# Kernel tuning notes

Hardware: AMD Instinct MI355X
Metric: run time of the kernel (lower is better)

## Reference

```python
import jax, jax.numpy as jnp
import numpy as np

B, S = 2, 1024
IN, OUT = 1024, 1024
N_IN, N_OUT = 32, 32          # isqrt(IN), isqrt(OUT)
CD = 64                       # compressed_feature_dim
K = 2                         # num_monarchs
D1 = N_IN * N_IN * N_OUT      # 32768, flat M1 size per token
D2 = N_OUT * N_IN * N_OUT     # 32768, flat M2 size per token


def setup_inputs() -> dict:
    key = jax.random.key(0)
    ks = jax.random.split(key, 13)
    g = lambda k, shape, s=0.02: jax.random.normal(k, shape, dtype=jnp.float32) * s
    return {
        "x":  jax.random.normal(ks[0], (B, S, IN), dtype=jnp.float32),
        "Wc": g(ks[1], (IN, CD)),  "bc": g(ks[2], (CD,)),
        "W1": g(ks[3], (K, CD, D1)), "b1": g(ks[4], (K, D1)),
        "W2": g(ks[5], (K, CD, D2)), "b2": g(ks[6], (K, D2)),
        "Wm": g(ks[7], (CD, K)),   "bm": g(ks[8], (K,)),
        "Wb": g(ks[9], (CD, OUT)), "bb": g(ks[10], (OUT,)),
        "Wr": g(ks[11], (CD, 1)),  "br": g(ks[12], (1,)),
    }


def reference(x, Wc, bc, W1, b1, W2, b2, Wm, bm, Wb, bb, Wr, br):
    b, s, _ = x.shape
    # compressor: Linear + Tanh -> [B,S,CD]
    cf = jnp.tanh(x @ Wc + bc)
    # per-expert generated flat weights: [B,S,K,D]
    gen1 = jnp.einsum('bsc,kcd->bskd', cf, W1) + b1
    gen2 = jnp.einsum('bsc,kcd->bskd', cf, W2) + b2
    # expert mixing coefficients -> softmax over K
    coeffs = jax.nn.softmax(cf @ Wm + bm, axis=-1)  # [B,S,K]
    M1f = jnp.einsum('bskd,bsk->bsd', gen1, coeffs)
    M2f = jnp.einsum('bskd,bsk->bsd', gen2, coeffs)
    # Monarch block matmul with per-token weights
    M1 = M1f.reshape(b, s, N_IN, N_IN, N_OUT)   # g=N_IN blocks of [N_IN,N_OUT]
    M2 = M2f.reshape(b, s, N_OUT, N_IN, N_OUT)  # g=N_OUT blocks of [N_IN,N_OUT]
    x1 = x.reshape(b, s, N_IN, N_IN)
    h1 = jnp.einsum('bsgi,bsgio->bsgo', x1, M1)      # [B,S,N_IN,N_OUT]
    h1t = jnp.swapaxes(h1, -1, -2)                   # [B,S,N_OUT,N_IN]
    h2 = jnp.einsum('bsgi,bsgio->bsgo', h1t, M2)     # [B,S,N_OUT,N_OUT]
    y = h2.reshape(b, s, OUT)
    # per-token scale and bias
    ratio = cf @ Wr + br                             # [B,S,1]
    bias = cf @ Wb + bb                              # [B,S,OUT]
    return y * ratio + bias
```

## Files before the change

### kernel.cpp

```cpp
#include <hip/hip_runtime.h>
#include <cstddef>

typedef unsigned short ushortT;
typedef short s8v __attribute__((ext_vector_type(8)));
typedef float f32x4 __attribute__((ext_vector_type(4)));

constexpr int NTOK = 2048;

__device__ inline ushortT f2bf(float f) {
  unsigned u = __float_as_uint(f);
  u += 0x7fffu + ((u >> 16) & 1u);
  return (ushortT)(u >> 16);
}

__global__ __launch_bounds__(256) void prep_kernel(
    const float* __restrict__ x, const float* __restrict__ Wc, const float* __restrict__ bc,
    const float* __restrict__ Wm, const float* __restrict__ bm,
    const float* __restrict__ Wr, const float* __restrict__ br,
    ushortT* __restrict__ FP, float* __restrict__ ratio)
{
  const int tid = threadIdx.x;
  const int c = tid & 63;
  const int q = tid >> 6;
  const int t0 = blockIdx.x * 8;
  __shared__ float part[4][8][64];
  __shared__ float cf_s[8][64];
  __shared__ float a0s[8], a1s[8];

  float acc[8];
#pragma unroll
  for (int p = 0; p < 8; ++p) acc[p] = 0.f;

  const float* xq = x + (size_t)t0 * 1024 + q * 256;
  const float* wq = Wc + (size_t)(q * 256) * 64 + c;
#pragma unroll 4
  for (int jj = 0; jj < 64; ++jj) {
    float w0 = wq[(jj * 4 + 0) * 64];
    float w1 = wq[(jj * 4 + 1) * 64];
    float w2 = wq[(jj * 4 + 2) * 64];
    float w3 = wq[(jj * 4 + 3) * 64];
#pragma unroll
    for (int p = 0; p < 8; ++p) {
      float4 xv = *(const float4*)(xq + (size_t)p * 1024 + jj * 4);
      acc[p] = fmaf(xv.x, w0, acc[p]);
      acc[p] = fmaf(xv.y, w1, acc[p]);
      acc[p] = fmaf(xv.z, w2, acc[p]);
      acc[p] = fmaf(xv.w, w3, acc[p]);
    }
  }
#pragma unroll
  for (int p = 0; p < 8; ++p) part[q][p][c] = acc[p];
  __syncthreads();

#pragma unroll
  for (int r = 0; r < 2; ++r) {
    int idx = tid + r * 256;
    int p = idx >> 6, cc = idx & 63;
    float s = part[0][p][cc] + part[1][p][cc] + part[2][p][cc] + part[3][p][cc] + bc[cc];
    cf_s[p][cc] = tanhf(s);
  }
  __syncthreads();

#pragma unroll 1
  for (int pp = 0; pp < 2; ++pp) {
    int p = q * 2 + pp;
    float cf = cf_s[p][c];
    float z0 = cf * Wm[2 * c], z1 = cf * Wm[2 * c + 1], rr = cf * Wr[c];
    for (int off = 32; off; off >>= 1) {
      z0 += __shfl_down(z0, off);
      z1 += __shfl_down(z1, off);
      rr += __shfl_down(rr, off);
    }
    if (c == 0) {
      z0 += bm[0]; z1 += bm[1];
      float mx = fmaxf(z0, z1);
      float e0 = expf(z0 - mx), e1 = expf(z1 - mx);
      float a0 = e0 / (e0 + e1);
      a0s[p] = a0;
      a1s[p] = 1.0f - a0;
      ratio[t0 + p] = rr + br[0];
    }
  }
  __syncthreads();

  const int ks0 = c >> 5, kk = c & 31;
  const int slot = (kk >> 3) * 16, e = kk & 7;
#pragma unroll
  for (int pp = 0; pp < 2; ++pp) {
    int p = q * 2 + pp;
    int t = t0 + p, tt = t >> 4, tok = t & 15;
    size_t base = (size_t)tt * 2560;
    float cf = cf_s[p][c];
    float a0 = a0s[p], a1 = a1s[p];
    FP[base + (size_t)ks0 * 512 + (slot + tok) * 8 + e]       = f2bf(a0 * cf);
    FP[base + (size_t)(2 + ks0) * 512 + (slot + tok) * 8 + e] = f2bf(a1 * cf);
    if (c < 32) {
      float v = (c == 0) ? a0 : (c == 1) ? a1 : 0.0f;
      FP[base + 4 * 512 + ((c >> 3) * 16 + tok) * 8 + (c & 7)] = f2bf(v);
    }
  }
}

__global__ __launch_bounds__(256) void pack_w_kernel(
    const float* __restrict__ W1, const float* __restrict__ b1,
    const float* __restrict__ W2, const float* __restrict__ b2,
    const float* __restrict__ Wb, const float* __restrict__ bb,
    ushortT* __restrict__ P1, ushortT* __restrict__ P2, ushortT* __restrict__ WbP)
{
  const int g = blockIdx.x, jc = blockIdx.y, fac = blockIdx.z;
  if (fac == 2 && g != 0) return;
  const float* W  = (fac == 0) ? W1 : W2;
  const float* bv = (fac == 0) ? b1 : b2;
  ushortT* P = (fac == 0) ? P1 : (fac == 1) ? P2 : WbP;
  const int tid = threadIdx.x;
  __shared__ ushortT lds[16][1024];

#pragma unroll
  for (int it = 0; it < 16; ++it) {
    int idx = tid + it * 256;
    int rl = idx >> 8, c4 = idx & 255;
    int jj = jc * 16 + rl;
    float4 v = make_float4(0.f, 0.f, 0.f, 0.f);
    if (fac < 2) {
      if (jj < 128)       v = *(const float4*)(W  + (size_t)jj * 32768 + g * 1024 + c4 * 4);
      else if (jj < 130)  v = *(const float4*)(bv + (size_t)(jj - 128) * 32768 + g * 1024 + c4 * 4);
    } else {
      if (jj < 128)       v = *(const float4*)(Wb + (size_t)(jj & 63) * 1024 + c4 * 4);
      else if (jj < 130)  v = *(const float4*)(bb + c4 * 4);
    }
    int col0 = c4 * 4;
    int sw = col0 ^ ((col0 >> 4) & 0x1C);
    ushortT* d = &lds[rl][sw];
    d[0] = f2bf(v.x); d[1] = f2bf(v.y); d[2] = f2bf(v.z); d[3] = f2bf(v.w);
  }
  __syncthreads();
  const int ks = jc >> 1, kh = jc & 1;
#pragma unroll
  for (int it = 0; it < 8; ++it) {
    int idx = tid + it * 256;
    int ct_l = idx >> 5, kkg_l = (idx >> 4) & 1, cl = idx & 15;
    int scol;
    if (fac < 2) {
      int o = ct_l >> 1, ib = (ct_l & 1) * 16;
      scol = (ib + cl) * 32 + o;
    } else {
      scol = ct_l * 16 + cl;
    }
    scol ^= ((scol >> 4) & 0x1C);
    int r0 = kkg_l * 8;
    ushortT v[8];
#pragma unroll
    for (int e = 0; e < 8; ++e) v[e] = lds[r0 + e][scol];
    int kkg = kh * 2 + kkg_l;
    size_t ctile = (fac < 2) ? (size_t)(g * 64 + ct_l) : (size_t)ct_l;
    size_t off = ctile * 2560 + (size_t)ks * 512 + (kkg * 16 + cl) * 8;
    uint4 qv;
    qv.x = v[0] | ((unsigned)v[1] << 16);
    qv.y = v[2] | ((unsigned)v[3] << 16);
    qv.z = v[4] | ((unsigned)v[5] << 16);
    qv.w = v[6] | ((unsigned)v[7] << 16);
    *(uint4*)(P + off) = qv;
  }
}

__global__ __launch_bounds__(256) void tr_kernel(
    const float* __restrict__ h1, float* __restrict__ h1x)
{
  __shared__ float lds[8 * 1061];
  const int tid = threadIdx.x, t0 = blockIdx.x * 8;
#pragma unroll
  for (int it = 0; it < 8; ++it) {
    int idx = tid + it * 256;
    int r = idx >> 8, c4 = idx & 255;
    float4 v = *(const float4*)(h1 + (size_t)(t0 + r) * 1024 + c4 * 4);
    int cc = c4 * 4, i = cc >> 5, b0 = cc & 31;
    float* d = lds + r * 1061 + i * 33 + b0;
    d[0] = v.x; d[1] = v.y; d[2] = v.z; d[3] = v.w;
  }
  __syncthreads();
#pragma unroll
  for (int it = 0; it < 8; ++it) {
    int idx = tid + it * 256;
    int g = idx >> 6, rest = idx & 63, r = rest >> 3, i4 = rest & 7;
    float4 v;
    v.x = lds[r * 1061 + (i4 * 4 + 0) * 33 + g];
    v.y = lds[r * 1061 + (i4 * 4 + 1) * 33 + g];
    v.z = lds[r * 1061 + (i4 * 4 + 2) * 33 + g];
    v.w = lds[r * 1061 + (i4 * 4 + 3) * 33 + g];
    *(float4*)(h1x + (size_t)g * 65536 + (size_t)(t0 + r) * 32 + i4 * 4) = v;
  }
}

template <int PASS>
__global__ __launch_bounds__(256, 2) void mm_kernel(
    const s8v* __restrict__ fP, const s8v* __restrict__ wP,
    const s8v* __restrict__ wbP,
    const float* __restrict__ xg,
    const float* __restrict__ rat,
    float* __restrict__ outp)
{
  __shared__ s8v bsh[2][1280];
  __shared__ float xs[2][64][33];
  __shared__ float hs[2][64][9];
  __shared__ float bls[2][64][9];
  const int tid = threadIdx.x;
  const int lane = tid & 63;
  const int w = tid >> 6;
  const int bid = blockIdx.x;
  const int cb  = (bid & 7) * 16 + (bid >> 6);
  const int tbg = (bid >> 3) & 7;
  const int g = cb >> 2;

  const s8v* ap = wP + (size_t)(cb * 16 + w * 4) * 320 + lane;
  s8v a[4][5];
#pragma unroll
  for (int i = 0; i < 4; ++i)
#pragma unroll
    for (int ks = 0; ks < 5; ++ks) a[i][ks] = ap[i * 320 + ks * 64];

  s8v ab[5];
  if (PASS == 2) {
    const s8v* abp = wbP + (size_t)(cb >> 1) * 320 + lane;
#pragma unroll
    for (int ks = 0; ks < 5; ++ks) ab[ks] = abp[ks * 64];
  }

  const s8v* fbase = fP + (size_t)(tbg * 4) * 1280;

#pragma unroll
  for (int it = 0; it < 5; ++it) bsh[0][tid + it * 256] = fbase[tid + it * 256];
  __syncthreads();

#pragma unroll 1
  for (int tt2 = 0; tt2 < 4; ++tt2) {
    const int buf = tt2 & 1;
    const int t0 = (tbg * 4 + tt2) * 64;

    float4 xv[2];
#pragma unroll
    for (int it = 0; it < 2; ++it) {
      int idx = tid + it * 256;
      int t = idx >> 3, i4 = idx & 7;
      if (PASS == 1) xv[it] = *(const float4*)(xg + (size_t)(t0 + t) * 1024 + g * 32 + i4 * 4);
      else           xv[it] = *(const float4*)(xg + (size_t)g * 65536 + (size_t)(t0 + t) * 32 + i4 * 4);
    }
    s8v st0, st1, st2, st3, st4;
    if (tt2 < 3) {
      const s8v* fn = fbase + (size_t)(tt2 + 1) * 1280;
      st0 = fn[tid];       st1 = fn[tid + 256]; st2 = fn[tid + 512];
      st3 = fn[tid + 768]; st4 = fn[tid + 1024];
    }

    f32x4 acc[4][4];
#pragma unroll
    for (int i = 0; i < 4; ++i)
#pragma unroll
      for (int j = 0; j < 4; ++j) acc[i][j] = {0.f, 0.f, 0.f, 0.f};
    f32x4 accb = {0.f, 0.f, 0.f, 0.f};

#pragma unroll
    for (int ks = 0; ks < 5; ++ks) {
      s8v b0 = bsh[buf][0 * 320 + ks * 64 + lane];
      s8v b1 = bsh[buf][1 * 320 + ks * 64 + lane];
      s8v b2 = bsh[buf][2 * 320 + ks * 64 + lane];
      s8v b3 = bsh[buf][3 * 320 + ks * 64 + lane];
      if (PASS == 2) {
        s8v bw = bsh[buf][w * 320 + ks * 64 + lane];
        accb = __builtin_amdgcn_mfma_f32_16x16x32_bf16(ab[ks], bw, accb, 0, 0, 0);
      }
#pragma unroll
      for (int i = 0; i < 4; ++i) {
        acc[i][0] = __builtin_amdgcn_mfma_f32_16x16x32_bf16(a[i][ks], b0, acc[i][0], 0, 0, 0);
        acc[i][1] = __builtin_amdgcn_mfma_f32_16x16x32_bf16(a[i][ks], b1, acc[i][1], 0, 0, 0);
        acc[i][2] = __builtin_amdgcn_mfma_f32_16x16x32_bf16(a[i][ks], b2, acc[i][2], 0, 0, 0);
        acc[i][3] = __builtin_amdgcn_mfma_f32_16x16x32_bf16(a[i][ks], b3, acc[i][3], 0, 0, 0);
      }
    }

#pragma unroll
    for (int it = 0; it < 2; ++it) {
      int idx = tid + it * 256;
      int t = idx >> 3, i4 = idx & 7;
      float* d = &xs[buf][t][i4 * 4];
      d[0] = xv[it].x; d[1] = xv[it].y; d[2] = xv[it].z; d[3] = xv[it].w;
    }
    if (tt2 < 3) {
      s8v* dn = &bsh[buf ^ 1][0];
      dn[tid] = st0;        dn[tid + 256] = st1; dn[tid + 512] = st2;
      dn[tid + 768] = st3;  dn[tid + 1024] = st4;
    }
    __syncthreads();

    const int tau = lane & 15, q = lane >> 4;
#pragma unroll
    for (int tt = 0; tt < 4; ++tt) {
      int tl = tt * 16 + tau;
#pragma unroll
      for (int run = 0; run < 2; ++run) {
        float sacc = 0.f;
#pragma unroll
        for (int ch = 0; ch < 2; ++ch) {
          int ct = run * 2 + ch;
          const float* xp = &xs[buf][tl][ch * 16 + q * 4];
          f32x4 av = acc[ct][tt];
          sacc += av[0] * xp[0] + av[1] * xp[1] + av[2] * xp[2] + av[3] * xp[3];
        }
        sacc += __shfl_xor(sacc, 16);
        sacc += __shfl_xor(sacc, 32);
        if (lane < 16) hs[buf][tl][w * 2 + run] = sacc;
      }
    }
    if (PASS == 2) {
      if ((lane >> 5) == (cb & 1)) {
        int ol = ((lane >> 4) & 1) * 4;
#pragma unroll
        for (int r = 0; r < 4; ++r) bls[buf][w * 16 + tau][ol + r] = accb[r];
      }
    }
    __syncthreads();

    if (tid < 128) {
      int row = tid >> 1, half = tid & 1;
      int t = t0 + row;
      int col = g * 32 + (cb & 3) * 8 + half * 4;
      float v0 = hs[buf][row][half * 4 + 0], v1 = hs[buf][row][half * 4 + 1];
      float v2 = hs[buf][row][half * 4 + 2], v3 = hs[buf][row][half * 4 + 3];
      float4 o;
      if (PASS == 2) {
        float r = rat[t];
        o.x = fmaf(v0, r, bls[buf][row][half * 4 + 0]);
        o.y = fmaf(v1, r, bls[buf][row][half * 4 + 1]);
        o.z = fmaf(v2, r, bls[buf][row][half * 4 + 2]);
        o.w = fmaf(v3, r, bls[buf][row][half * 4 + 3]);
      } else {
        o.x = v0; o.y = v1; o.z = v2; o.w = v3;
      }
      *(float4*)(outp + (size_t)t * 1024 + col) = o;
    }
  }
}

extern "C" void kernel_launch(void* const* d_in, const int* in_sizes, int n_in,
                              void* d_out, int out_size, void* d_ws, size_t ws_size,
                              hipStream_t stream) {
  const float* x  = (const float*)d_in[0];
  const float* Wc = (const float*)d_in[1];
  const float* bc = (const float*)d_in[2];
  const float* W1 = (const float*)d_in[3];
  const float* b1 = (const float*)d_in[4];
  const float* W2 = (const float*)d_in[5];
  const float* b2 = (const float*)d_in[6];
  const float* Wm = (const float*)d_in[7];
  const float* bm = (const float*)d_in[8];
  const float* Wb = (const float*)d_in[9];
  const float* bb = (const float*)d_in[10];
  const float* Wr = (const float*)d_in[11];
  const float* br = (const float*)d_in[12];
  float* out = (float*)d_out;

  ushortT* P1  = (ushortT*)d_ws;
  ushortT* P2  = P1 + (size_t)2048 * 2560;
  ushortT* WbP = P2 + (size_t)2048 * 2560;
  ushortT* FP  = WbP + (size_t)64 * 2560;
  float* ratio = (float*)(FP + (size_t)128 * 2560);
  float* h1    = ratio + NTOK;
  float* h1x   = h1 + (size_t)NTOK * 1024;

  prep_kernel<<<dim3(256), dim3(256), 0, stream>>>(x, Wc, bc, Wm, bm, Wr, br, FP, ratio);
  pack_w_kernel<<<dim3(32, 10, 3), dim3(256), 0, stream>>>(W1, b1, W2, b2, Wb, bb, P1, P2, WbP);
  mm_kernel<1><<<dim3(1024), dim3(256), 0, stream>>>(
      (const s8v*)FP, (const s8v*)P1, (const s8v*)WbP, x, nullptr, h1);
  tr_kernel<<<dim3(256), dim3(256), 0, stream>>>(h1, h1x);
  mm_kernel<2><<<dim3(1024), dim3(256), 0, stream>>>(
      (const s8v*)FP, (const s8v*)P2, (const s8v*)WbP, h1x, ratio, out);
}
```

Measured before the change: 95.32 us.

## Merge prep and pack kernels, prefetch B tiles with direct global-to-LDS loads

Combines the token prep kernel and the weight packing kernel into a single launch with block-range dispatch, and trims the empty fac=2 blocks from the grid. In the matmul kernel, the next B tile is now staged with global_load_lds builtins straight into the alternate LDS buffer instead of going through registers. The double-buffered xs/hs/bls arrays become single-buffered, which lowers LDS use. The goal is less launch overhead, fewer registers and less LDS traffic. The cost is a more complex kernel, and the async LDS writes depend on the existing barriers for correct ordering.

Result: slower. 98.09 us (+2.9%).

```diff
diff --git a/kernel.cpp b/kernel.cpp
--- a/kernel.cpp
+++ b/kernel.cpp
@@ -13,153 +13,163 @@
   return (ushortT)(u >> 16);
 }
 
-__global__ __launch_bounds__(256) void prep_kernel(
+__device__ inline void gl_lds16(const s8v* g, s8v* l) {
+  __builtin_amdgcn_global_load_lds(
+      (const __attribute__((address_space(1))) unsigned int*)g,
+      (__attribute__((address_space(3))) unsigned int*)l, 16, 0, 0);
+}
+
+__global__ __launch_bounds__(256) void setup_kernel(
     const float* __restrict__ x, const float* __restrict__ Wc, const float* __restrict__ bc,
     const float* __restrict__ Wm, const float* __restrict__ bm,
     const float* __restrict__ Wr, const float* __restrict__ br,
-    ushortT* __restrict__ FP, float* __restrict__ ratio)
-{
-  const int tid = threadIdx.x;
-  const int c = tid & 63;
-  const int q = tid >> 6;
-  const int t0 = blockIdx.x * 8;
-  __shared__ float part[4][8][64];
-  __shared__ float cf_s[8][64];
-  __shared__ float a0s[8], a1s[8];
-
-  float acc[8];
-#pragma unroll
-  for (int p = 0; p < 8; ++p) acc[p] = 0.f;
-
-  const float* xq = x + (size_t)t0 * 1024 + q * 256;
-  const float* wq = Wc + (size_t)(q * 256) * 64 + c;
-#pragma unroll 4
-  for (int jj = 0; jj < 64; ++jj) {
-    float w0 = wq[(jj * 4 + 0) * 64];
-    float w1 = wq[(jj * 4 + 1) * 64];
-    float w2 = wq[(jj * 4 + 2) * 64];
-    float w3 = wq[(jj * 4 + 3) * 64];
-#pragma unroll
-    for (int p = 0; p < 8; ++p) {
-      float4 xv = *(const float4*)(xq + (size_t)p * 1024 + jj * 4);
-      acc[p] = fmaf(xv.x, w0, acc[p]);
-      acc[p] = fmaf(xv.y, w1, acc[p]);
-      acc[p] = fmaf(xv.z, w2, acc[p]);
-      acc[p] = fmaf(xv.w, w3, acc[p]);
-    }
-  }
-#pragma unroll
-  for (int p = 0; p < 8; ++p) part[q][p][c] = acc[p];
-  __syncthreads();
-
-#pragma unroll
-  for (int r = 0; r < 2; ++r) {
-    int idx = tid + r * 256;
-    int p = idx >> 6, cc = idx & 63;
-    float s = part[0][p][cc] + part[1][p][cc] + part[2][p][cc] + part[3][p][cc] + bc[cc];
-    cf_s[p][cc] = tanhf(s);
-  }
-  __syncthreads();
-
-#pragma unroll 1
-  for (int pp = 0; pp < 2; ++pp) {
-    int p = q * 2 + pp;
-    float cf = cf_s[p][c];
-    float z0 = cf * Wm[2 * c], z1 = cf * Wm[2 * c + 1], rr = cf * Wr[c];
-    for (int off = 32; off; off >>= 1) {
-      z0 += __shfl_down(z0, off);
-      z1 += __shfl_down(z1, off);
-      rr += __shfl_down(rr, off);
-    }
-    if (c == 0) {
-      z0 += bm[0]; z1 += bm[1];
-      float mx = fmaxf(z0, z1);
-      float e0 = expf(z0 - mx), e1 = expf(z1 - mx);
-      float a0 = e0 / (e0 + e1);
-      a0s[p] = a0;
-      a1s[p] = 1.0f - a0;
-      ratio[t0 + p] = rr + br[0];
-    }
-  }
-  __syncthreads();
-
-  const int ks0 = c >> 5, kk = c & 31;
-  const int slot = (kk >> 3) * 16, e = kk & 7;
-#pragma unroll
-  for (int pp = 0; pp < 2; ++pp) {
-    int p = q * 2 + pp;
-    int t = t0 + p, tt = t >> 4, tok = t & 15;
-    size_t base = (size_t)tt * 2560;
-    float cf = cf_s[p][c];
-    float a0 = a0s[p], a1 = a1s[p];
-    FP[base + (size_t)ks0 * 512 + (slot + tok) * 8 + e]       = f2bf(a0 * cf);
-    FP[base + (size_t)(2 + ks0) * 512 + (slot + tok) * 8 + e] = f2bf(a1 * cf);
-    if (c < 32) {
-      float v = (c == 0) ? a0 : (c == 1) ? a1 : 0.0f;
-      FP[base + 4 * 512 + ((c >> 3) * 16 + tok) * 8 + (c & 7)] = f2bf(v);
-    }
-  }
-}
-
-__global__ __launch_bounds__(256) void pack_w_kernel(
     const float* __restrict__ W1, const float* __restrict__ b1,
     const float* __restrict__ W2, const float* __restrict__ b2,
     const float* __restrict__ Wb, const float* __restrict__ bb,
+    ushortT* __restrict__ FP, float* __restrict__ ratio,
     ushortT* __restrict__ P1, ushortT* __restrict__ P2, ushortT* __restrict__ WbP)
 {
-  const int g = blockIdx.x, jc = blockIdx.y, fac = blockIdx.z;
-  if (fac == 2 && g != 0) return;
-  const float* W  = (fac == 0) ? W1 : W2;
-  const float* bv = (fac == 0) ? b1 : b2;
-  ushortT* P = (fac == 0) ? P1 : (fac == 1) ? P2 : WbP;
+  __shared__ __align__(16) char smem[32768];
   const int tid = threadIdx.x;
-  __shared__ ushortT lds[16][1024];
-
-#pragma unroll
-  for (int it = 0; it < 16; ++it) {
-    int idx = tid + it * 256;
-    int rl = idx >> 8, c4 = idx & 255;
-    int jj = jc * 16 + rl;
-    float4 v = make_float4(0.f, 0.f, 0.f, 0.f);
-    if (fac < 2) {
-      if (jj < 128)       v = *(const float4*)(W  + (size_t)jj * 32768 + g * 1024 + c4 * 4);
-      else if (jj < 130)  v = *(const float4*)(bv + (size_t)(jj - 128) * 32768 + g * 1024 + c4 * 4);
-    } else {
-      if (jj < 128)       v = *(const float4*)(Wb + (size_t)(jj & 63) * 1024 + c4 * 4);
-      else if (jj < 130)  v = *(const float4*)(bb + c4 * 4);
-    }
-    int col0 = c4 * 4;
-    int sw = col0 ^ ((col0 >> 4) & 0x1C);
-    ushortT* d = &lds[rl][sw];
-    d[0] = f2bf(v.x); d[1] = f2bf(v.y); d[2] = f2bf(v.z); d[3] = f2bf(v.w);
-  }
-  __syncthreads();
-  const int ks = jc >> 1, kh = jc & 1;
-#pragma unroll
-  for (int it = 0; it < 8; ++it) {
-    int idx = tid + it * 256;
-    int ct_l = idx >> 5, kkg_l = (idx >> 4) & 1, cl = idx & 15;
-    int scol;
-    if (fac < 2) {
-      int o = ct_l >> 1, ib = (ct_l & 1) * 16;
-      scol = (ib + cl) * 32 + o;
-    } else {
-      scol = ct_l * 16 + cl;
-    }
-    scol ^= ((scol >> 4) & 0x1C);
-    int r0 = kkg_l * 8;
-    ushortT v[8];
-#pragma unroll
-    for (int e = 0; e < 8; ++e) v[e] = lds[r0 + e][scol];
-    int kkg = kh * 2 + kkg_l;
-    size_t ctile = (fac < 2) ? (size_t)(g * 64 + ct_l) : (size_t)ct_l;
-    size_t off = ctile * 2560 + (size_t)ks * 512 + (kkg * 16 + cl) * 8;
-    uint4 qv;
-    qv.x = v[0] | ((unsigned)v[1] << 16);
-    qv.y = v[2] | ((unsigned)v[3] << 16);
-    qv.z = v[4] | ((unsigned)v[5] << 16);
-    qv.w = v[6] | ((unsigned)v[7] << 16);
-    *(uint4*)(P + off) = qv;
+  const int bid = blockIdx.x;
+
+  if (bid < 256) {
+    float* part = (float*)smem;
+    float* cf_s = part + 2048;
+    float* a0s  = cf_s + 512;
+    float* a1s  = a0s + 8;
+    const int c = tid & 63;
+    const int q = tid >> 6;
+    const int t0 = bid * 8;
+
+    float acc[8];
+#pragma unroll
+    for (int p = 0; p < 8; ++p) acc[p] = 0.f;
+    const float* xq = x + (size_t)t0 * 1024 + q * 256;
+    const float* wq = Wc + (size_t)(q * 256) * 64 + c;
+#pragma unroll 4
+    for (int jj = 0; jj < 64; ++jj) {
+      float w0 = wq[(jj * 4 + 0) * 64];
+      float w1 = wq[(jj * 4 + 1) * 64];
+      float w2 = wq[(jj * 4 + 2) * 64];
+      float w3 = wq[(jj * 4 + 3) * 64];
+#pragma unroll
+      for (int p = 0; p < 8; ++p) {
+        float4 xv = *(const float4*)(xq + (size_t)p * 1024 + jj * 4);
+        acc[p] = fmaf(xv.x, w0, acc[p]);
+        acc[p] = fmaf(xv.y, w1, acc[p]);
+        acc[p] = fmaf(xv.z, w2, acc[p]);
+        acc[p] = fmaf(xv.w, w3, acc[p]);
+      }
+    }
+#pragma unroll
+    for (int p = 0; p < 8; ++p) part[(q * 8 + p) * 64 + c] = acc[p];
+    __syncthreads();
+
+#pragma unroll
+    for (int r = 0; r < 2; ++r) {
+      int idx = tid + r * 256;
+      int p = idx >> 6, cc = idx & 63;
+      float s = part[(0 * 8 + p) * 64 + cc] + part[(1 * 8 + p) * 64 + cc] +
+                part[(2 * 8 + p) * 64 + cc] + part[(3 * 8 + p) * 64 + cc] + bc[cc];
+      cf_s[p * 64 + cc] = tanhf(s);
+    }
+    __syncthreads();
+
+#pragma unroll 1
+    for (int pp = 0; pp < 2; ++pp) {
+      int p = q * 2 + pp;
+      float cf = cf_s[p * 64 + c];
+      float z0 = cf * Wm[2 * c], z1 = cf * Wm[2 * c + 1], rr = cf * Wr[c];
+      for (int off = 32; off; off >>= 1) {
+        z0 += __shfl_down(z0, off);
+        z1 += __shfl_down(z1, off);
+        rr += __shfl_down(rr, off);
+      }
+      if (c == 0) {
+        z0 += bm[0]; z1 += bm[1];
+        float mx = fmaxf(z0, z1);
+        float e0 = expf(z0 - mx), e1 = expf(z1 - mx);
+        float a0 = e0 / (e0 + e1);
+        a0s[p] = a0;
+        a1s[p] = 1.0f - a0;
+        ratio[t0 + p] = rr + br[0];
+      }
+    }
+    __syncthreads();
+
+    const int ks0 = c >> 5, kk = c & 31;
+    const int slot = (kk >> 3) * 16, e = kk & 7;
+#pragma unroll
+    for (int pp = 0; pp < 2; ++pp) {
+      int p = q * 2 + pp;
+      int t = t0 + p, tt = t >> 4, tok = t & 15;
+      size_t base = (size_t)tt * 2560;
+      float cf = cf_s[p * 64 + c];
+      float a0 = a0s[p], a1 = a1s[p];
+      FP[base + (size_t)ks0 * 512 + (slot + tok) * 8 + e]       = f2bf(a0 * cf);
+      FP[base + (size_t)(2 + ks0) * 512 + (slot + tok) * 8 + e] = f2bf(a1 * cf);
+      if (c < 32) {
+        float v = (c == 0) ? a0 : (c == 1) ? a1 : 0.0f;
+        FP[base + 4 * 512 + ((c >> 3) * 16 + tok) * 8 + (c & 7)] = f2bf(v);
+      }
+    }
+  } else {
+    ushortT (*lds)[1024] = (ushortT (*)[1024])smem;
+    int pb = bid - 256;
+    int fac, g, jc;
+    if (pb < 640) { fac = pb / 320; int rem = pb % 320; g = rem / 10; jc = rem % 10; }
+    else          { fac = 2; g = 0; jc = pb - 640; }
+    const float* W  = (fac == 0) ? W1 : W2;
+    const float* bv = (fac == 0) ? b1 : b2;
+    ushortT* P = (fac == 0) ? P1 : (fac == 1) ? P2 : WbP;
+
+#pragma unroll
+    for (int it = 0; it < 16; ++it) {
+      int idx = tid + it * 256;
+      int rl = idx >> 8, c4 = idx & 255;
+      int jj = jc * 16 + rl;
+      float4 v = make_float4(0.f, 0.f, 0.f, 0.f);
+      if (fac < 2) {
+        if (jj < 128)       v = *(const float4*)(W  + (size_t)jj * 32768 + g * 1024 + c4 * 4);
+        else if (jj < 130)  v = *(const float4*)(bv + (size_t)(jj - 128) * 32768 + g * 1024 + c4 * 4);
+      } else {
+        if (jj < 128)       v = *(const float4*)(Wb + (size_t)(jj & 63) * 1024 + c4 * 4);
+        else if (jj < 130)  v = *(const float4*)(bb + c4 * 4);
+      }
+      int col0 = c4 * 4;
+      int sw = col0 ^ ((col0 >> 4) & 0x1C);
+      ushortT* d = &lds[rl][sw];
+      d[0] = f2bf(v.x); d[1] = f2bf(v.y); d[2] = f2bf(v.z); d[3] = f2bf(v.w);
+    }
+    __syncthreads();
+    const int ks = jc >> 1, kh = jc & 1;
+#pragma unroll
+    for (int it = 0; it < 8; ++it) {
+      int idx = tid + it * 256;
+      int ct_l = idx >> 5, kkg_l = (idx >> 4) & 1, cl = idx & 15;
+      int scol;
+      if (fac < 2) {
+        int o = ct_l >> 1, ib = (ct_l & 1) * 16;
+        scol = (ib + cl) * 32 + o;
+      } else {
+        scol = ct_l * 16 + cl;
+      }
+      scol ^= ((scol >> 4) & 0x1C);
+      int r0 = kkg_l * 8;
+      ushortT v[8];
+#pragma unroll
+      for (int e = 0; e < 8; ++e) v[e] = lds[r0 + e][scol];
+      int kkg = kh * 2 + kkg_l;
+      size_t ctile = (fac < 2) ? (size_t)(g * 64 + ct_l) : (size_t)ct_l;
+      size_t off = ctile * 2560 + (size_t)ks * 512 + (kkg * 16 + cl) * 8;
+      uint4 qv;
+      qv.x = v[0] | ((unsigned)v[1] << 16);
+      qv.y = v[2] | ((unsigned)v[3] << 16);
+      qv.z = v[4] | ((unsigned)v[5] << 16);
+      qv.w = v[6] | ((unsigned)v[7] << 16);
+      *(uint4*)(P + off) = qv;
+    }
   }
 }
 
@@ -200,9 +210,9 @@
     float* __restrict__ outp)
 {
   __shared__ s8v bsh[2][1280];
-  __shared__ float xs[2][64][33];
-  __shared__ float hs[2][64][9];
-  __shared__ float bls[2][64][9];
+  __shared__ float xs[64][33];
+  __shared__ float hs[64][9];
+  __shared__ float bls[PASS == 2 ? 64 : 1][9];
   const int tid = threadIdx.x;
   const int lane = tid & 63;
   const int w = tid >> 6;
@@ -219,7 +229,7 @@
     for (int ks = 0; ks < 5; ++ks) a[i][ks] = ap[i * 320 + ks * 64];
 
   s8v ab[5];
-  if (PASS == 2) {
+  if constexpr (PASS == 2) {
     const s8v* abp = wbP + (size_t)(cb >> 1) * 320 + lane;
 #pragma unroll
     for (int ks = 0; ks < 5; ++ks) ab[ks] = abp[ks * 64];
@@ -228,7 +238,8 @@
   const s8v* fbase = fP + (size_t)(tbg * 4) * 1280;
 
 #pragma unroll
-  for (int it = 0; it < 5; ++it) bsh[0][tid + it * 256] = fbase[tid + it * 256];
+  for (int c2 = 0; c2 < 5; ++c2)
+    gl_lds16(fbase + w * 320 + c2 * 64 + lane, &bsh[0][w * 320 + c2 * 64]);
   __syncthreads();
 
 #pragma unroll 1
@@ -244,11 +255,11 @@
       if (PASS == 1) xv[it] = *(const float4*)(xg + (size_t)(t0 + t) * 1024 + g * 32 + i4 * 4);
       else           xv[it] = *(const float4*)(xg + (size_t)g * 65536 + (size_t)(t0 + t) * 32 + i4 * 4);
     }
-    s8v st0, st1, st2, st3, st4;
     if (tt2 < 3) {
       const s8v* fn = fbase + (size_t)(tt2 + 1) * 1280;
-      st0 = fn[tid];       st1 = fn[tid + 256]; st2 = fn[tid + 512];
-      st3 = fn[tid + 768]; st4 = fn[tid + 1024];
+#pragma unroll
+      for (int c2 = 0; c2 < 5; ++c2)
+        gl_lds16(fn + w * 320 + c2 * 64 + lane, &bsh[buf ^ 1][w * 320 + c2 * 64]);
     }
 
     f32x4 acc[4][4];
@@ -264,7 +275,7 @@
       s8v b1 = bsh[buf][1 * 320 + ks * 64 + lane];
       s8v b2 = bsh[buf][2 * 320 + ks * 64 + lane];
       s8v b3 = bsh[buf][3 * 320 + ks * 64 + lane];
-      if (PASS == 2) {
+      if constexpr (PASS == 2) {
         s8v bw = bsh[buf][w * 320 + ks * 64 + lane];
         accb = __builtin_amdgcn_mfma_f32_16x16x32_bf16(ab[ks], bw, accb, 0, 0, 0);
       }
@@ -281,13 +292,8 @@
     for (int it = 0; it < 2; ++it) {
       int idx = tid + it * 256;
       int t = idx >> 3, i4 = idx & 7;
-      float* d = &xs[buf][t][i4 * 4];
+      float* d = &xs[t][i4 * 4];
       d[0] = xv[it].x; d[1] = xv[it].y; d[2] = xv[it].z; d[3] = xv[it].w;
-    }
-    if (tt2 < 3) {
-      s8v* dn = &bsh[buf ^ 1][0];
-      dn[tid] = st0;        dn[tid + 256] = st1; dn[tid + 512] = st2;
-      dn[tid + 768] = st3;  dn[tid + 1024] = st4;
     }
     __syncthreads();
 
@@ -301,20 +307,20 @@
 #pragma unroll
         for (int ch = 0; ch < 2; ++ch) {
           int ct = run * 2 + ch;
-          const float* xp = &xs[buf][tl][ch * 16 + q * 4];
+          const float* xp = &xs[tl][ch * 16 + q * 4];
           f32x4 av = acc[ct][tt];
           sacc += av[0] * xp[0] + av[1] * xp[1] + av[2] * xp[2] + av[3] * xp[3];
         }
         sacc += __shfl_xor(sacc, 16);
         sacc += __shfl_xor(sacc, 32);
-        if (lane < 16) hs[buf][tl][w * 2 + run] = sacc;
-      }
-    }
-    if (PASS == 2) {
+        if (lane < 16) hs[tl][w * 2 + run] = sacc;
+      }
+    }
+    if constexpr (PASS == 2) {
       if ((lane >> 5) == (cb & 1)) {
         int ol = ((lane >> 4) & 1) * 4;
 #pragma unroll
-        for (int r = 0; r < 4; ++r) bls[buf][w * 16 + tau][ol + r] = accb[r];
+        for (int r = 0; r < 4; ++r) bls[w * 16 + tau][ol + r] = accb[r];
       }
     }
     __syncthreads();
@@ -323,15 +329,15 @@
       int row = tid >> 1, half = tid & 1;
       int t = t0 + row;
       int col = g * 32 + (cb & 3) * 8 + half * 4;
-      float v0 = hs[buf][row][half * 4 + 0], v1 = hs[buf][row][half * 4 + 1];
-      float v2 = hs[buf][row][half * 4 + 2], v3 = hs[buf][row][half * 4 + 3];
+      float v0 = hs[row][half * 4 + 0], v1 = hs[row][half * 4 + 1];
+      float v2 = hs[row][half * 4 + 2], v3 = hs[row][half * 4 + 3];
       float4 o;
-      if (PASS == 2) {
+      if constexpr (PASS == 2) {
         float r = rat[t];
-        o.x = fmaf(v0, r, bls[buf][row][half * 4 + 0]);
-        o.y = fmaf(v1, r, bls[buf][row][half * 4 + 1]);
-        o.z = fmaf(v2, r, bls[buf][row][half * 4 + 2]);
-        o.w = fmaf(v3, r, bls[buf][row][half * 4 + 3]);
+        o.x = fmaf(v0, r, bls[row][half * 4 + 0]);
+        o.y = fmaf(v1, r, bls[row][half * 4 + 1]);
+        o.z = fmaf(v2, r, bls[row][half * 4 + 2]);
+        o.w = fmaf(v3, r, bls[row][half * 4 + 3]);
       } else {
         o.x = v0; o.y = v1; o.z = v2; o.w = v3;
       }
@@ -366,8 +372,8 @@
   float* h1    = ratio + NTOK;
   float* h1x   = h1 + (size_t)NTOK * 1024;
 
-  prep_kernel<<<dim3(256), dim3(256), 0, stream>>>(x, Wc, bc, Wm, bm, Wr, br, FP, ratio);
-  pack_w_kernel<<<dim3(32, 10, 3), dim3(256), 0, stream>>>(W1, b1, W2, b2, Wb, bb, P1, P2, WbP);
+  setup_kernel<<<dim3(906), dim3(256), 0, stream>>>(
+      x, Wc, bc, Wm, bm, Wr, br, W1, b1, W2, b2, Wb, bb, FP, ratio, P1, P2, WbP);
   mm_kernel<1><<<dim3(1024), dim3(256), 0, stream>>>(
       (const s8v*)FP, (const s8v*)P1, (const s8v*)WbP, x, nullptr, h1);
   tr_kernel<<<dim3(256), dim3(256), 0, stream>>>(h1, h1x);
```
